# Kernel tuning notes

Measured on AMD Instinct MI355X. Metric: run time of the kernel, lower is better.

The kernel has to match this reference:

```python
import jax, jax.numpy as jnp
import numpy as np

B, NS, NC = 4096, 1024, 256
GUMBEL_HARD = True


def _linear(x, W, b):
    # torch nn.Linear: y = x @ W.T + b, W is [out, in]
    return x @ W.T + b


def _gumbel_softmax(logits, gnoise, tau, hard):
    y = jax.nn.softmax((logits + gnoise) / tau, axis=-1)
    if hard:
        y_hard = jax.nn.one_hot(jnp.argmax(y, axis=-1), y.shape[-1], dtype=y.dtype)
        y = y_hard + y - jax.lax.stop_gradient(y)  # straight-through
    return y


def setup_inputs() -> dict:
    key = jax.random.key(0)
    ks = jax.random.split(key, 32)
    inp = {
        "ct": jax.random.normal(ks[0], (B, NC), jnp.float32),
        "b1": jax.random.uniform(ks[1], (B, 2), jnp.float32),
        "b2": jax.random.uniform(ks[2], (B, 2), jnp.float32),
        "b3": jax.random.uniform(ks[3], (B, 2), jnp.float32),
        "rnn1": jax.random.normal(ks[4], (B, NS), jnp.float32),
        "rnn2": jax.random.normal(ks[5], (B, NS), jnp.float32),
        "rnn3": jax.random.normal(ks[6], (B, NS), jnp.float32),
        "rnn4": jax.random.normal(ks[7], (B, NS), jnp.float32),
        "gn1": jax.random.gumbel(ks[8], (B, 2), jnp.float32),
        "gn2": jax.random.gumbel(ks[9], (B, 2), jnp.float32),
        "gn3": jax.random.gumbel(ks[10], (B, 2), jnp.float32),
        "theta": 1,
    }
    def lin(k, out_d, in_d):
        return (0.02 * jax.random.normal(k, (out_d, in_d), jnp.float32),
                jnp.zeros((out_d,), jnp.float32))
    shapes = {
        "e_ct": (NS, NC), "rnn1_b0": (NS, 2 * NS), "rnn1_b1": (NS, 2 * NS),
        "b1_rnn1": (2, NS), "rnn2_b0": (NS, 2 * NS), "rnn2_b1": (NS, 2 * NS),
        "b2_rnn2": (2, NS), "rnn3_b0": (NS, 2 * NS), "rnn3_b1": (NS, 2 * NS),
        "b3_rnn3": (2, NS), "rnn4": (NS, 2 * NS), "hg_rnns": (NS, 4 * NS),
        "g_hg": (4, NS), "hctpi_rnns": (NS, 4 * NS), "ctpi_hctpi": (NC, NS),
    }
    for i, (name, (o, ii)) in enumerate(shapes.items()):
        W, bb = lin(ks[11 + i], o, ii)
        inp["W_" + name] = W
        inp["b_" + name] = bb
    return inp


def reference(ct, b1, b2, b3, rnn1, rnn2, rnn3, rnn4, gn1, gn2, gn3, theta,
              W_e_ct, b_e_ct, W_rnn1_b0, b_rnn1_b0, W_rnn1_b1, b_rnn1_b1,
              W_b1_rnn1, b_b1_rnn1, W_rnn2_b0, b_rnn2_b0, W_rnn2_b1, b_rnn2_b1,
              W_b2_rnn2, b_b2_rnn2, W_rnn3_b0, b_rnn3_b0, W_rnn3_b1, b_rnn3_b1,
              W_b3_rnn3, b_b3_rnn3, W_rnn4, b_rnn4, W_hg_rnns, b_hg_rnns,
              W_g_hg, b_g_hg, W_hctpi_rnns, b_hctpi_rnns, W_ctpi_hctpi, b_ctpi_hctpi):
    tau = jnp.float32(theta)
    b1tm1f = b1[:, 0:1]
    ct_e = jax.nn.relu(_linear(ct, W_e_ct, b_e_ct))

    rnn1b1 = jnp.tanh(_linear(jnp.concatenate((rnn2, ct_e), axis=1), W_rnn1_b1, b_rnn1_b1))
    rnn1b0 = jnp.tanh(_linear(jnp.concatenate((rnn1, ct_e), axis=1), W_rnn1_b0, b_rnn1_b0))
    rnn1t = b1tm1f * rnn1b1 + (1.0 - b1tm1f) * rnn1b0
    b1t = _gumbel_softmax(_linear(rnn1t, W_b1_rnn1, b_b1_rnn1), gn1, tau, GUMBEL_HARD)
    b1tf = b1t[:, 0:1]

    b2tm1f = b2[:, 0:1]
    rnn2b1 = jnp.tanh(_linear(jnp.concatenate((rnn3, rnn1t), axis=1), W_rnn2_b1, b_rnn2_b1))
    rnn2b0 = jnp.tanh(_linear(jnp.concatenate((rnn2, rnn1t), axis=1), W_rnn2_b0, b_rnn2_b0))
    rnn2_inner = (1.0 - b2tm1f) * rnn2b0 + b2tm1f * rnn2b1
    rnn2t = (1.0 - b1tf) * rnn2 + b1tf * rnn2_inner
    b2tnew = _gumbel_softmax(_linear(rnn2t, W_b2_rnn2, b_b2_rnn2), gn2, tau, GUMBEL_HARD)
    b2t = b1tf * b2tnew + (1.0 - b1tf) * b2
    b2tf = b2t[:, 0:1]

    b3tm1f = b3[:, 0:1]
    rnn3b1 = jnp.tanh(_linear(jnp.concatenate((rnn4, rnn2t), axis=1), W_rnn3_b1, b_rnn3_b1))
    rnn3b0 = jnp.tanh(_linear(jnp.concatenate((rnn3, rnn2t), axis=1), W_rnn3_b0, b_rnn3_b0))
    rnn3_inner = b3tm1f * rnn3b1 + (1.0 - b3tm1f) * rnn3b0
    rnn3t = (1.0 - b1tf) * rnn3 + b1tf * ((1.0 - b2tf) * rnn3 + b2tf * rnn3_inner)
    b3tnew = _gumbel_softmax(_linear(rnn3t, W_b3_rnn3, b_b3_rnn3), gn3, tau, GUMBEL_HARD)
    b3t = b1tf * (b2tf * b3tnew + (1.0 - b2tf) * b3) + (1.0 - b1tf) * b3
    b3tf = b3t[:, 0:1]

    rnn4_inner = jnp.tanh(_linear(jnp.concatenate((rnn4, rnn3t), axis=1), W_rnn4, b_rnn4))
    rnn4t = (1.0 - b1tf) * rnn4 + b1tf * ((1.0 - b2tf) * rnn4 + b2tf * ((1.0 - b3tf) * rnn4 + b3tf * rnn4_inner))

    hg = jax.nn.relu(_linear(jnp.concatenate((rnn1t, rnn2t, rnn3t, rnn4t), axis=1), W_hg_rnns, b_hg_rnns))
    g = jax.nn.sigmoid(_linear(hg, W_g_hg, b_g_hg))
    gated = jnp.concatenate((g[:, 0:1] * rnn1t, g[:, 1:2] * rnn2t, g[:, 2:3] * rnn3t, g[:, 3:4] * rnn4t), axis=1)
    hctpi = jax.nn.relu(_linear(gated, W_hctpi_rnns, b_hctpi_rnns))
    ctpi = jax.nn.log_softmax(_linear(hctpi, W_ctpi_hctpi, b_ctpi_hctpi), axis=1)
    return (ctpi, b1t, b2t, b3t, rnn1t, rnn2t, rnn3t, rnn4t)
```

## Files before the change

kernel.cpp:

```cpp
#include <hip/hip_runtime.h>
#include <cstdint>
#include <cstddef>

typedef unsigned short u16;
typedef __bf16 bf16x8 __attribute__((ext_vector_type(8)));
typedef float  f32x4  __attribute__((ext_vector_type(4)));

__device__ __forceinline__ void splitv(const float4 a, const float4 b, bf16x8& h, bf16x8& l) {
    float x[8] = {a.x, a.y, a.z, a.w, b.x, b.y, b.z, b.w};
#pragma unroll
    for (int i = 0; i < 8; i++) {
        __bf16 hh = (__bf16)x[i];
        h[i] = hh;
        l[i] = (__bf16)(x[i] - (float)hh);
    }
}
__device__ __forceinline__ void hiv(const float4 a, const float4 b, bf16x8& h) {
    float x[8] = {a.x, a.y, a.z, a.w, b.x, b.y, b.z, b.w};
#pragma unroll
    for (int i = 0; i < 8; i++) h[i] = (__bf16)x[i];
}

struct GemmArgs {
    const float* A0[4];
    const float* A1[4];
    const float* B0; const float* B1;
    const float* bias0; const float* bias1;
    float* Z0; float* Z1;
    int bk[4];
    int nsec, lda, ldb, N, spsl, relu, npass;
};

__global__ __launch_bounds__(256, 4) void gemm_v2(GemmArgs p) {
    __shared__ u16 Ah[128 * 32];
    __shared__ u16 Al[128 * 32];
    __shared__ u16 Bh[64 * 32];
    __shared__ u16 Bl[64 * 32];
    const int tid = threadIdx.x;
    const int lin = blockIdx.x;
    const int mt = ((lin & 7) << 2) | ((lin >> 3) & 3);
    const int nt = lin >> 5;
    const int NTh = p.N >> 6;
    const int half = (nt >= NTh) ? 1 : 0;
    const int n0 = (nt - (half ? NTh : 0)) * 64;
    const int m0 = mt * 128;
    const float* Bw  = half ? p.B1 : p.B0;
    const float* bia = half ? p.bias1 : p.bias0;
    float* Z         = half ? p.Z1 : p.Z0;
    const float* const* Asec = half ? p.A1 : p.A0;

    const int wave = tid >> 6, lane = tid & 63;
    const int quad = lane >> 4, lr = lane & 15;
    const int wm = (wave & 1) * 64, wn = (wave >> 1) * 32;
    const bool np3 = (p.npass == 3);

    f32x4 acc[4][2];
#pragma unroll
    for (int i = 0; i < 4; i++)
#pragma unroll
        for (int j = 0; j < 2; j++) acc[i][j] = (f32x4){0.f, 0.f, 0.f, 0.f};

    const int arow = tid >> 2;
    const int acol = (tid & 3) * 8;
    const size_t rA0 = (size_t)(m0 + arow) * p.lda + acol;
    const size_t rA1 = rA0 + (size_t)64 * p.lda;
    const size_t rB  = (size_t)(n0 + arow) * p.ldb + acol;
    const int sps = 1 << p.spsl;
    const int total = p.nsec << p.spsl;

    float4 v0a, v0b, v1a, v1b, vba, vbb;
    {
        const float* Ag = Asec[0];
        const float* a0 = Ag + rA0;
        const float* a1 = Ag + rA1;
        const float* b  = Bw + rB + p.bk[0];
        v0a = ((const float4*)a0)[0]; v0b = ((const float4*)a0)[1];
        v1a = ((const float4*)a1)[0]; v1b = ((const float4*)a1)[1];
        vba = ((const float4*)b)[0];  vbb = ((const float4*)b)[1];
    }

    for (int tt = 0; tt < total; ++tt) {
        __syncthreads();
        bf16x8 h, l;
        if (np3) {
            splitv(v0a, v0b, h, l);
            *(bf16x8*)&Ah[tid * 8] = h;        *(bf16x8*)&Al[tid * 8] = l;
            splitv(v1a, v1b, h, l);
            *(bf16x8*)&Ah[2048 + tid * 8] = h; *(bf16x8*)&Al[2048 + tid * 8] = l;
            splitv(vba, vbb, h, l);
            *(bf16x8*)&Bh[tid * 8] = h;        *(bf16x8*)&Bl[tid * 8] = l;
        } else {
            hiv(v0a, v0b, h); *(bf16x8*)&Ah[tid * 8] = h;
            hiv(v1a, v1b, h); *(bf16x8*)&Ah[2048 + tid * 8] = h;
            hiv(vba, vbb, h); *(bf16x8*)&Bh[tid * 8] = h;
        }
        __syncthreads();
        if (tt + 1 < total) {
            const int ts = tt + 1;
            const int s = ts >> p.spsl, t = ts & (sps - 1);
            const float* Ag = Asec[s];
            const float* a0 = Ag + rA0 + t * 32;
            const float* a1 = Ag + rA1 + t * 32;
            const float* b  = Bw + rB + p.bk[s] + t * 32;
            v0a = ((const float4*)a0)[0]; v0b = ((const float4*)a0)[1];
            v1a = ((const float4*)a1)[0]; v1b = ((const float4*)a1)[1];
            vba = ((const float4*)b)[0];  vbb = ((const float4*)b)[1];
        }
        bf16x8 ah[4], bh2[2];
#pragma unroll
        for (int i = 0; i < 4; i++)
            ah[i] = *reinterpret_cast<const bf16x8*>(&Ah[(wm + i * 16 + lr) * 32 + quad * 8]);
#pragma unroll
        for (int j = 0; j < 2; j++)
            bh2[j] = *reinterpret_cast<const bf16x8*>(&Bh[(wn + j * 16 + lr) * 32 + quad * 8]);
#pragma unroll
        for (int i = 0; i < 4; i++)
#pragma unroll
            for (int j = 0; j < 2; j++)
                acc[i][j] = __builtin_amdgcn_mfma_f32_16x16x32_bf16(ah[i], bh2[j], acc[i][j], 0, 0, 0);
        if (np3) {
            bf16x8 al[4], bl2[2];
#pragma unroll
            for (int i = 0; i < 4; i++)
                al[i] = *reinterpret_cast<const bf16x8*>(&Al[(wm + i * 16 + lr) * 32 + quad * 8]);
#pragma unroll
            for (int j = 0; j < 2; j++)
                bl2[j] = *reinterpret_cast<const bf16x8*>(&Bl[(wn + j * 16 + lr) * 32 + quad * 8]);
#pragma unroll
            for (int i = 0; i < 4; i++)
#pragma unroll
                for (int j = 0; j < 2; j++) {
                    acc[i][j] = __builtin_amdgcn_mfma_f32_16x16x32_bf16(ah[i], bl2[j], acc[i][j], 0, 0, 0);
                    acc[i][j] = __builtin_amdgcn_mfma_f32_16x16x32_bf16(al[i], bh2[j], acc[i][j], 0, 0, 0);
                }
        }
    }

#pragma unroll
    for (int j = 0; j < 2; j++) {
        const int n = n0 + wn + j * 16 + lr;
        const float bj = bia[n];
#pragma unroll
        for (int i = 0; i < 4; i++)
#pragma unroll
            for (int r = 0; r < 4; r++) {
                const int m = m0 + wm + i * 16 + quad * 4 + r;
                float v = acc[i][j][r] + bj;
                if (p.relu) v = fmaxf(v, 0.f);
                Z[(size_t)m * p.N + n] = v;
            }
    }
}

__global__ __launch_bounds__(256) void combine1(const float* Z0, const float* Z1, const float* b1in,
                                                float* outr) {
    const int base = (blockIdx.x * 256 + threadIdx.x) * 4;
    const int m = base >> 10;
    const float bf = b1in[2 * m];
    const float4 z0 = *(const float4*)(Z0 + base), z1 = *(const float4*)(Z1 + base);
    float4 o;
    o.x = bf * tanhf(z1.x) + (1.f - bf) * tanhf(z0.x);
    o.y = bf * tanhf(z1.y) + (1.f - bf) * tanhf(z0.y);
    o.z = bf * tanhf(z1.z) + (1.f - bf) * tanhf(z0.z);
    o.w = bf * tanhf(z1.w) + (1.f - bf) * tanhf(z0.w);
    *(float4*)(outr + base) = o;
}
__global__ __launch_bounds__(256) void combine2(const float* Z0, const float* Z1, const float* b2in,
                                                const float* rnn2in, const float* F1, float* outr) {
    const int base = (blockIdx.x * 256 + threadIdx.x) * 4;
    const int m = base >> 10;
    const float b2f = b2in[2 * m], f1 = F1[m];
    const float4 z0 = *(const float4*)(Z0 + base), z1 = *(const float4*)(Z1 + base);
    const float4 r2 = *(const float4*)(rnn2in + base);
    float4 o;
    o.x = (1.f - f1) * r2.x + f1 * ((1.f - b2f) * tanhf(z0.x) + b2f * tanhf(z1.x));
    o.y = (1.f - f1) * r2.y + f1 * ((1.f - b2f) * tanhf(z0.y) + b2f * tanhf(z1.y));
    o.z = (1.f - f1) * r2.z + f1 * ((1.f - b2f) * tanhf(z0.z) + b2f * tanhf(z1.z));
    o.w = (1.f - f1) * r2.w + f1 * ((1.f - b2f) * tanhf(z0.w) + b2f * tanhf(z1.w));
    *(float4*)(outr + base) = o;
}
__global__ __launch_bounds__(256) void combine3(const float* Z0, const float* Z1, const float* b3in,
                                                const float* rnn3in, const float* F1, const float* F2,
                                                float* outr) {
    const int base = (blockIdx.x * 256 + threadIdx.x) * 4;
    const int m = base >> 10;
    const float b3f = b3in[2 * m], f1 = F1[m], f2 = F2[m];
    const float4 z0 = *(const float4*)(Z0 + base), z1 = *(const float4*)(Z1 + base);
    const float4 r3 = *(const float4*)(rnn3in + base);
    float4 o;
    o.x = (1.f - f1) * r3.x + f1 * ((1.f - f2) * r3.x + f2 * (b3f * tanhf(z1.x) + (1.f - b3f) * tanhf(z0.x)));
    o.y = (1.f - f1) * r3.y + f1 * ((1.f - f2) * r3.y + f2 * (b3f * tanhf(z1.y) + (1.f - b3f) * tanhf(z0.y)));
    o.z = (1.f - f1) * r3.z + f1 * ((1.f - f2) * r3.z + f2 * (b3f * tanhf(z1.z) + (1.f - b3f) * tanhf(z0.z)));
    o.w = (1.f - f1) * r3.w + f1 * ((1.f - f2) * r3.w + f2 * (b3f * tanhf(z1.w) + (1.f - b3f) * tanhf(z0.w)));
    *(float4*)(outr + base) = o;
}
__global__ __launch_bounds__(256) void combine4(const float* Z0, const float* rnn4in, const float* F1,
                                                const float* F2, const float* F3, float* outr) {
    const int base = (blockIdx.x * 256 + threadIdx.x) * 4;
    const int m = base >> 10;
    const float f1 = F1[m], f2 = F2[m], f3 = F3[m];
    const float4 z0 = *(const float4*)(Z0 + base);
    const float4 r4 = *(const float4*)(rnn4in + base);
    float4 o;
    o.x = (1.f - f1) * r4.x + f1 * ((1.f - f2) * r4.x + f2 * ((1.f - f3) * r4.x + f3 * tanhf(z0.x)));
    o.y = (1.f - f1) * r4.y + f1 * ((1.f - f2) * r4.y + f2 * ((1.f - f3) * r4.y + f3 * tanhf(z0.y)));
    o.z = (1.f - f1) * r4.z + f1 * ((1.f - f2) * r4.z + f2 * ((1.f - f3) * r4.z + f3 * tanhf(z0.z)));
    o.w = (1.f - f1) * r4.w + f1 * ((1.f - f2) * r4.w + f2 * ((1.f - f3) * r4.w + f3 * tanhf(z0.w)));
    *(float4*)(outr + base) = o;
}

__global__ __launch_bounds__(256) void gemv_decide(const float* x, const float* W2, const float* bias2,
                                                   const float* gn, const float* bprev,
                                                   const float* Fp1, const float* Fp2,
                                                   float* bout, float* fout, int stage) {
    const int wave = threadIdx.x >> 6, lane = threadIdx.x & 63;
    const int m = blockIdx.x * 4 + wave;
    const float* row = x + (size_t)m * 1024;
    float s0 = 0.f, s1 = 0.f;
#pragma unroll 4
    for (int i = 0; i < 16; i++) {
        const int k = lane + 64 * i;
        const float v = row[k];
        s0 += v * W2[k];
        s1 += v * W2[1024 + k];
    }
    for (int off = 32; off > 0; off >>= 1) { s0 += __shfl_xor(s0, off); s1 += __shfl_xor(s1, off); }
    if (lane == 0) {
        const float l0 = s0 + bias2[0] + gn[2 * m];
        const float l1 = s1 + bias2[1] + gn[2 * m + 1];
        const float nf = (l0 >= l1) ? 1.f : 0.f;
        float v0, v1;
        if (stage == 1) {
            v0 = nf; v1 = 1.f - nf;
        } else if (stage == 2) {
            const float f1 = Fp1[m];
            const float p0 = bprev[2 * m], p1 = bprev[2 * m + 1];
            v0 = f1 * nf + (1.f - f1) * p0;
            v1 = f1 * (1.f - nf) + (1.f - f1) * p1;
        } else {
            const float f1 = Fp1[m], f2 = Fp2[m];
            const float p0 = bprev[2 * m], p1 = bprev[2 * m + 1];
            const float i0 = f2 * nf + (1.f - f2) * p0;
            const float i1 = f2 * (1.f - nf) + (1.f - f2) * p1;
            v0 = f1 * i0 + (1.f - f1) * p0;
            v1 = f1 * i1 + (1.f - f1) * p1;
        }
        fout[m] = v0;
        bout[2 * m] = v0; bout[2 * m + 1] = v1;
    }
}

__global__ __launch_bounds__(256) void gemv_g4(const float* hg, const float* Wg, const float* bg, float* G) {
    const int wave = threadIdx.x >> 6, lane = threadIdx.x & 63;
    const int m = blockIdx.x * 4 + wave;
    const float* row = hg + (size_t)m * 1024;
    float s[4] = {0.f, 0.f, 0.f, 0.f};
#pragma unroll 4
    for (int i = 0; i < 16; i++) {
        const int k = lane + 64 * i;
        const float v = row[k];
#pragma unroll
        for (int j = 0; j < 4; j++) s[j] += v * Wg[j * 1024 + k];
    }
    for (int off = 32; off > 0; off >>= 1)
#pragma unroll
        for (int j = 0; j < 4; j++) s[j] += __shfl_xor(s[j], off);
    if (lane == 0) {
#pragma unroll
        for (int j = 0; j < 4; j++) G[m * 4 + j] = 1.f / (1.f + expf(-(s[j] + bg[j])));
    }
}

__global__ __launch_bounds__(256) void gated_k(const float* rnnF, const float* G, float* gated) {
    const int base = (blockIdx.x * 256 + threadIdx.x) * 4;
    const int m = base >> 12, rem = base & 4095;
    const int j = rem >> 10, k = rem & 1023;
    const float g = G[m * 4 + j];
    const float4 r = *(const float4*)(rnnF + (size_t)j * 4194304 + (size_t)m * 1024 + k);
    float4 o; o.x = g * r.x; o.y = g * r.y; o.z = g * r.z; o.w = g * r.w;
    *(float4*)(gated + base) = o;
}

__global__ __launch_bounds__(256) void logsoftmax_k(const float* Z, float* out) {
    const int wave = threadIdx.x >> 6, lane = threadIdx.x & 63;
    const int row = blockIdx.x * 4 + wave;
    const size_t base = (size_t)row * 256;
    float x[4];
#pragma unroll
    for (int i = 0; i < 4; i++) x[i] = Z[base + lane + 64 * i];
    float mx = fmaxf(fmaxf(x[0], x[1]), fmaxf(x[2], x[3]));
    for (int off = 32; off > 0; off >>= 1) mx = fmaxf(mx, __shfl_xor(mx, off));
    float s = 0.f;
#pragma unroll
    for (int i = 0; i < 4; i++) s += expf(x[i] - mx);
    for (int off = 32; off > 0; off >>= 1) s += __shfl_xor(s, off);
    const float lse = mx + logf(s);
#pragma unroll
    for (int i = 0; i < 4; i++) out[base + lane + 64 * i] = x[i] - lse;
}

static const size_t OUT_B1 = 1048576, OUT_B2 = 1056768, OUT_B3 = 1064960;
static const size_t OUT_R1 = 1073152, OUT_R2 = 5267456, OUT_R3 = 9461760, OUT_R4 = 13656064;

extern "C" void kernel_launch(void* const* d_in, const int* in_sizes, int n_in,
                              void* d_out, int out_size, void* d_ws, size_t ws_size,
                              hipStream_t stream) {
    (void)in_sizes; (void)n_in; (void)out_size; (void)ws_size;
    const float* ct   = (const float*)d_in[0];
    const float* b1   = (const float*)d_in[1];
    const float* b2   = (const float*)d_in[2];
    const float* b3   = (const float*)d_in[3];
    const float* rnn1 = (const float*)d_in[4];
    const float* rnn2 = (const float*)d_in[5];
    const float* rnn3 = (const float*)d_in[6];
    const float* rnn4 = (const float*)d_in[7];
    const float* gn1  = (const float*)d_in[8];
    const float* gn2  = (const float*)d_in[9];
    const float* gn3  = (const float*)d_in[10];
    const float* W_e    = (const float*)d_in[12]; const float* be    = (const float*)d_in[13];
    const float* W_r1b0 = (const float*)d_in[14]; const float* br1b0 = (const float*)d_in[15];
    const float* W_r1b1 = (const float*)d_in[16]; const float* br1b1 = (const float*)d_in[17];
    const float* W_b1   = (const float*)d_in[18]; const float* bb1   = (const float*)d_in[19];
    const float* W_r2b0 = (const float*)d_in[20]; const float* br2b0 = (const float*)d_in[21];
    const float* W_r2b1 = (const float*)d_in[22]; const float* br2b1 = (const float*)d_in[23];
    const float* W_b2   = (const float*)d_in[24]; const float* bb2   = (const float*)d_in[25];
    const float* W_r3b0 = (const float*)d_in[26]; const float* br3b0 = (const float*)d_in[27];
    const float* W_r3b1 = (const float*)d_in[28]; const float* br3b1 = (const float*)d_in[29];
    const float* W_b3   = (const float*)d_in[30]; const float* bb3   = (const float*)d_in[31];
    const float* W_r4   = (const float*)d_in[32]; const float* br4   = (const float*)d_in[33];
    const float* W_hg   = (const float*)d_in[34]; const float* bhg   = (const float*)d_in[35];
    const float* W_g    = (const float*)d_in[36]; const float* bg    = (const float*)d_in[37];
    const float* W_hct  = (const float*)d_in[38]; const float* bhct  = (const float*)d_in[39];
    const float* W_ct   = (const float*)d_in[40]; const float* bct   = (const float*)d_in[41];

    float* out = (float*)d_out;
    char* w = (char*)d_ws;
    const size_t MB = 1024 * 1024;
    float* Z0    = (float*)(w + 0 * MB);
    float* Z1    = (float*)(w + 16 * MB);
    float* CTEF  = (float*)(w + 32 * MB);
    float* HGF   = (float*)(w + 48 * MB);
    float* GATED = (float*)(w + 0 * MB);
    float* HCTF  = (float*)(w + 64 * MB);
    float* ZC    = (float*)(w + 0 * MB);
    float* F1 = out; float* F2 = F1 + 4096; float* F3 = F1 + 8192; float* G4 = F1 + 12288;
    float* R1 = out + OUT_R1; float* R2 = out + OUT_R2;
    float* R3 = out + OUT_R3; float* R4 = out + OUT_R4;

    auto gemm = [&](const float* a00, const float* a01, const float* a02, const float* a03,
                    const float* a10, const float* a11,
                    const float* B0w, const float* B1w, const float* bi0, const float* bi1,
                    float* z0, float* z1, int bk1, int bk2, int bk3,
                    int nsec, int lda, int ldb, int N, int spsl, int relu, int npass, int NT) {
        GemmArgs p;
        p.A0[0] = a00; p.A0[1] = a01; p.A0[2] = a02; p.A0[3] = a03;
        p.A1[0] = a10 ? a10 : a00; p.A1[1] = a11 ? a11 : a01; p.A1[2] = a02; p.A1[3] = a03;
        p.B0 = B0w; p.B1 = B1w; p.bias0 = bi0; p.bias1 = bi1; p.Z0 = z0; p.Z1 = z1;
        p.bk[0] = 0; p.bk[1] = bk1; p.bk[2] = bk2; p.bk[3] = bk3;
        p.nsec = nsec; p.lda = lda; p.ldb = ldb; p.N = N; p.spsl = spsl;
        p.relu = relu; p.npass = npass;
        gemm_v2<<<dim3(NT * 32), 256, 0, stream>>>(p);
    };
    const dim3 EW(4096), GV(1024);

    gemm(ct, 0, 0, 0, 0, 0, W_e, W_e, be, be, CTEF, CTEF,
         0, 0, 0, 1, 256, 256, 1024, 3, 1, 3, 16);
    gemm(rnn1, CTEF, 0, 0, rnn2, CTEF, W_r1b0, W_r1b1, br1b0, br1b1, Z0, Z1,
         1024, 0, 0, 2, 1024, 2048, 1024, 5, 0, 3, 32);
    combine1<<<EW, 256, 0, stream>>>(Z0, Z1, b1, R1);
    gemv_decide<<<GV, 256, 0, stream>>>(R1, W_b1, bb1, gn1, b1, F1, F1, out + OUT_B1, F1, 1);
    gemm(rnn2, R1, 0, 0, rnn3, R1, W_r2b0, W_r2b1, br2b0, br2b1, Z0, Z1,
         1024, 0, 0, 2, 1024, 2048, 1024, 5, 0, 3, 32);
    combine2<<<EW, 256, 0, stream>>>(Z0, Z1, b2, rnn2, F1, R2);
    gemv_decide<<<GV, 256, 0, stream>>>(R2, W_b2, bb2, gn2, b2, F1, F1, out + OUT_B2, F2, 2);
    gemm(rnn3, R2, 0, 0, rnn4, R2, W_r3b0, W_r3b1, br3b0, br3b1, Z0, Z1,
         1024, 0, 0, 2, 1024, 2048, 1024, 5, 0, 3, 32);
    combine3<<<EW, 256, 0, stream>>>(Z0, Z1, b3, rnn3, F1, F2, R3);
    gemv_decide<<<GV, 256, 0, stream>>>(R3, W_b3, bb3, gn3, b3, F1, F2, out + OUT_B3, F3, 3);
    gemm(rnn4, R3, 0, 0, 0, 0, W_r4, W_r4, br4, br4, Z0, Z0,
         1024, 0, 0, 2, 1024, 2048, 1024, 5, 0, 1, 16);
    combine4<<<EW, 256, 0, stream>>>(Z0, rnn4, F1, F2, F3, R4);
    gemm(R1, R2, R3, R4, 0, 0, W_hg, W_hg, bhg, bhg, HGF, HGF,
         1024, 2048, 3072, 4, 1024, 4096, 1024, 5, 1, 1, 16);
    gemv_g4<<<GV, 256, 0, stream>>>(HGF, W_g, bg, G4);
    gated_k<<<dim3(16384), 256, 0, stream>>>(R1, G4, GATED);
    gemm(GATED, 0, 0, 0, 0, 0, W_hct, W_hct, bhct, bhct, HCTF, HCTF,
         0, 0, 0, 1, 4096, 4096, 1024, 7, 1, 1, 16);
    gemm(HCTF, 0, 0, 0, 0, 0, W_ct, W_ct, bct, bct, ZC, ZC,
         0, 0, 0, 1, 1024, 1024, 256, 5, 0, 1, 4);
    logsoftmax_k<<<GV, 256, 0, stream>>>(ZC, out);
}
```

Baseline: 1.002 ms.

## Pre-split weights and activations to bf16 hi/lo and load via global_load_lds

Adds a conversion kernel that splits fp32 weights into bf16 hi/lo arrays before each GEMM. Combine, gated and GEMM epilogues now also emit bf16 (hi/lo) copies of activations. The GEMM loads these pre-converted operands straight into swizzled LDS with global_load_lds, so it no longer converts B and most A tiles in registers every K-step and moves half the bytes. The cost is extra conversion launches and extra traffic on every call for the weights, plus a more complex mixed-mode A path.

```diff
diff --git a/kernel.cpp b/kernel.cpp
--- a/kernel.cpp
+++ b/kernel.cpp
@@ -5,6 +5,7 @@
 typedef unsigned short u16;
 typedef __bf16 bf16x8 __attribute__((ext_vector_type(8)));
 typedef float  f32x4  __attribute__((ext_vector_type(4)));
+typedef u16    u16x4  __attribute__((ext_vector_type(4)));
 
 __device__ __forceinline__ void splitv(const float4 a, const float4 b, bf16x8& h, bf16x8& l) {
     float x[8] = {a.x, a.y, a.z, a.w, b.x, b.y, b.z, b.w};
@@ -21,21 +22,32 @@
     for (int i = 0; i < 8; i++) h[i] = (__bf16)x[i];
 }
 
+__device__ __forceinline__ void gl16(const void* g, void* l) {
+    __builtin_amdgcn_global_load_lds((__attribute__((address_space(1))) void*)g,
+                                     (__attribute__((address_space(3))) void*)l, 16, 0, 0);
+}
+
+struct Sec {
+    const void* h;
+    const u16*  l;
+    int lda; int mode;
+};
 struct GemmArgs {
-    const float* A0[4];
-    const float* A1[4];
-    const float* B0; const float* B1;
+    Sec A0[4]; Sec A1[4];
+    const u16* B0h; const u16* B0l;
+    const u16* B1h; const u16* B1l;
     const float* bias0; const float* bias1;
     float* Z0; float* Z1;
+    u16* Zh0; u16* Zl0; u16* Zh1; u16* Zl1;
     int bk[4];
-    int nsec, lda, ldb, N, spsl, relu, npass;
+    int nsec, ldb, N, spsl, relu, npass, zmode;
 };
 
-__global__ __launch_bounds__(256, 4) void gemm_v2(GemmArgs p) {
-    __shared__ u16 Ah[128 * 32];
-    __shared__ u16 Al[128 * 32];
-    __shared__ u16 Bh[64 * 32];
-    __shared__ u16 Bl[64 * 32];
+__global__ __launch_bounds__(256, 4) void gemm_v3(GemmArgs p) {
+    __shared__ __align__(16) u16 Ah[128 * 32];
+    __shared__ __align__(16) u16 Al[128 * 32];
+    __shared__ __align__(16) u16 Bh[64 * 32];
+    __shared__ __align__(16) u16 Bl[64 * 32];
     const int tid = threadIdx.x;
     const int lin = blockIdx.x;
     const int mt = ((lin & 7) << 2) | ((lin >> 3) & 3);
@@ -44,10 +56,13 @@
     const int half = (nt >= NTh) ? 1 : 0;
     const int n0 = (nt - (half ? NTh : 0)) * 64;
     const int m0 = mt * 128;
-    const float* Bw  = half ? p.B1 : p.B0;
+    const u16* Bwh = half ? p.B1h : p.B0h;
+    const u16* Bwl = half ? p.B1l : p.B0l;
     const float* bia = half ? p.bias1 : p.bias0;
-    float* Z         = half ? p.Z1 : p.Z0;
-    const float* const* Asec = half ? p.A1 : p.A0;
+    float* Z = half ? p.Z1 : p.Z0;
+    u16* Zh = half ? p.Zh1 : p.Zh0;
+    u16* Zl = half ? p.Zl1 : p.Zl0;
+    const Sec* As = half ? p.A1 : p.A0;
 
     const int wave = tid >> 6, lane = tid & 63;
     const int quad = lane >> 4, lr = lane & 15;
@@ -61,58 +76,79 @@
         for (int j = 0; j < 2; j++) acc[i][j] = (f32x4){0.f, 0.f, 0.f, 0.f};
 
     const int arow = tid >> 2;
-    const int acol = (tid & 3) * 8;
-    const size_t rA0 = (size_t)(m0 + arow) * p.lda + acol;
-    const size_t rA1 = rA0 + (size_t)64 * p.lda;
-    const size_t rB  = (size_t)(n0 + arow) * p.ldb + acol;
+    const int aslot = tid & 3;
+    const int csw = aslot ^ ((arow ^ (arow >> 2)) & 3);
+    const int wr_i0 = arow * 32 + csw * 8;
+    char* AhB = (char*)Ah; char* AlB = (char*)Al;
+    char* BhB = (char*)Bh; char* BlB = (char*)Bl;
+    const int ldsw = wave * 1024;
+
+    const int qx8 = ((quad ^ ((lr ^ (lr >> 2)) & 3)) & 3) * 8;
+
     const int sps = 1 << p.spsl;
     const int total = p.nsec << p.spsl;
 
-    float4 v0a, v0b, v1a, v1b, vba, vbb;
-    {
-        const float* Ag = Asec[0];
-        const float* a0 = Ag + rA0;
-        const float* a1 = Ag + rA1;
-        const float* b  = Bw + rB + p.bk[0];
-        v0a = ((const float4*)a0)[0]; v0b = ((const float4*)a0)[1];
-        v1a = ((const float4*)a1)[0]; v1b = ((const float4*)a1)[1];
-        vba = ((const float4*)b)[0];  vbb = ((const float4*)b)[1];
+    float4 v0a{}, v0b{}, v1a{}, v1b{};
+    {
+        const Sec s0 = As[0];
+        if (s0.mode == 0) {
+            const float* a0 = (const float*)s0.h + (size_t)(m0 + arow) * s0.lda + aslot * 8;
+            v0a = ((const float4*)a0)[0]; v0b = ((const float4*)a0)[1];
+            const float* a1 = a0 + (size_t)64 * s0.lda;
+            v1a = ((const float4*)a1)[0]; v1b = ((const float4*)a1)[1];
+        }
     }
 
     for (int tt = 0; tt < total; ++tt) {
+        const int s = tt >> p.spsl, t = tt & (sps - 1);
         __syncthreads();
-        bf16x8 h, l;
-        if (np3) {
-            splitv(v0a, v0b, h, l);
-            *(bf16x8*)&Ah[tid * 8] = h;        *(bf16x8*)&Al[tid * 8] = l;
-            splitv(v1a, v1b, h, l);
-            *(bf16x8*)&Ah[2048 + tid * 8] = h; *(bf16x8*)&Al[2048 + tid * 8] = l;
-            splitv(vba, vbb, h, l);
-            *(bf16x8*)&Bh[tid * 8] = h;        *(bf16x8*)&Bl[tid * 8] = l;
+        {
+            const size_t off = (size_t)(n0 + arow) * p.ldb + p.bk[s] + t * 32 + csw * 8;
+            gl16(Bwh + off, BhB + ldsw);
+            if (np3) gl16(Bwl + off, BlB + ldsw);
+        }
+        const Sec sec = As[s];
+        if (sec.mode == 0) {
+            if (np3) {
+                bf16x8 h, l;
+                splitv(v0a, v0b, h, l);
+                *(bf16x8*)&Ah[wr_i0] = h;        *(bf16x8*)&Al[wr_i0] = l;
+                splitv(v1a, v1b, h, l);
+                *(bf16x8*)&Ah[2048 + wr_i0] = h; *(bf16x8*)&Al[2048 + wr_i0] = l;
+            } else {
+                bf16x8 h;
+                hiv(v0a, v0b, h); *(bf16x8*)&Ah[wr_i0] = h;
+                hiv(v1a, v1b, h); *(bf16x8*)&Ah[2048 + wr_i0] = h;
+            }
         } else {
-            hiv(v0a, v0b, h); *(bf16x8*)&Ah[tid * 8] = h;
-            hiv(v1a, v1b, h); *(bf16x8*)&Ah[2048 + tid * 8] = h;
-            hiv(vba, vbb, h); *(bf16x8*)&Bh[tid * 8] = h;
+            const u16* gh = (const u16*)sec.h;
+            const size_t o0 = (size_t)(m0 + arow) * sec.lda + t * 32 + csw * 8;
+            const size_t o1 = o0 + (size_t)64 * sec.lda;
+            gl16(gh + o0, AhB + ldsw);
+            gl16(gh + o1, AhB + 4096 + ldsw);
+            if (np3) {
+                gl16(sec.l + o0, AlB + ldsw);
+                gl16(sec.l + o1, AlB + 4096 + ldsw);
+            }
         }
         __syncthreads();
         if (tt + 1 < total) {
-            const int ts = tt + 1;
-            const int s = ts >> p.spsl, t = ts & (sps - 1);
-            const float* Ag = Asec[s];
-            const float* a0 = Ag + rA0 + t * 32;
-            const float* a1 = Ag + rA1 + t * 32;
-            const float* b  = Bw + rB + p.bk[s] + t * 32;
-            v0a = ((const float4*)a0)[0]; v0b = ((const float4*)a0)[1];
-            v1a = ((const float4*)a1)[0]; v1b = ((const float4*)a1)[1];
-            vba = ((const float4*)b)[0];  vbb = ((const float4*)b)[1];
+            const int s2 = (tt + 1) >> p.spsl, t2 = (tt + 1) & (sps - 1);
+            const Sec sn = As[s2];
+            if (sn.mode == 0) {
+                const float* a0 = (const float*)sn.h + (size_t)(m0 + arow) * sn.lda + t2 * 32 + aslot * 8;
+                v0a = ((const float4*)a0)[0]; v0b = ((const float4*)a0)[1];
+                const float* a1 = a0 + (size_t)64 * sn.lda;
+                v1a = ((const float4*)a1)[0]; v1b = ((const float4*)a1)[1];
+            }
         }
         bf16x8 ah[4], bh2[2];
 #pragma unroll
         for (int i = 0; i < 4; i++)
-            ah[i] = *reinterpret_cast<const bf16x8*>(&Ah[(wm + i * 16 + lr) * 32 + quad * 8]);
+            ah[i] = *reinterpret_cast<const bf16x8*>(&Ah[(wm + i * 16 + lr) * 32 + qx8]);
 #pragma unroll
         for (int j = 0; j < 2; j++)
-            bh2[j] = *reinterpret_cast<const bf16x8*>(&Bh[(wn + j * 16 + lr) * 32 + quad * 8]);
+            bh2[j] = *reinterpret_cast<const bf16x8*>(&Bh[(wn + j * 16 + lr) * 32 + qx8]);
 #pragma unroll
         for (int i = 0; i < 4; i++)
 #pragma unroll
@@ -122,10 +158,10 @@
             bf16x8 al[4], bl2[2];
 #pragma unroll
             for (int i = 0; i < 4; i++)
-                al[i] = *reinterpret_cast<const bf16x8*>(&Al[(wm + i * 16 + lr) * 32 + quad * 8]);
+                al[i] = *reinterpret_cast<const bf16x8*>(&Al[(wm + i * 16 + lr) * 32 + qx8]);
 #pragma unroll
             for (int j = 0; j < 2; j++)
-                bl2[j] = *reinterpret_cast<const bf16x8*>(&Bl[(wn + j * 16 + lr) * 32 + quad * 8]);
+                bl2[j] = *reinterpret_cast<const bf16x8*>(&Bl[(wn + j * 16 + lr) * 32 + qx8]);
 #pragma unroll
             for (int i = 0; i < 4; i++)
 #pragma unroll
@@ -147,13 +183,46 @@
                 const int m = m0 + wm + i * 16 + quad * 4 + r;
                 float v = acc[i][j][r] + bj;
                 if (p.relu) v = fmaxf(v, 0.f);
-                Z[(size_t)m * p.N + n] = v;
+                const size_t zi = (size_t)m * p.N + n;
+                if (p.zmode == 0) {
+                    Z[zi] = v;
+                } else {
+                    __bf16 hb = (__bf16)v;
+                    Zh[zi] = __builtin_bit_cast(u16, hb);
+                    if (p.zmode == 2)
+                        Zl[zi] = __builtin_bit_cast(u16, (__bf16)(v - (float)hb));
+                }
             }
     }
 }
 
+__global__ __launch_bounds__(256) void conv_split(const float* x0, u16* h0, u16* l0, int n0v,
+                                                  const float* x1, u16* h1, u16* l1, int n1v) {
+    int i = blockIdx.x * 256 + threadIdx.x;
+    const float* x; u16* h; u16* l;
+    if (i < n0v) { x = x0; h = h0; l = l0; }
+    else { i -= n0v; if (i >= n1v) return; x = x1; h = h1; l = l1; }
+    const float4 a = ((const float4*)x)[2 * i], b = ((const float4*)x)[2 * i + 1];
+    bf16x8 hh, ll;
+    if (l) { splitv(a, b, hh, ll); ((bf16x8*)h)[i] = hh; ((bf16x8*)l)[i] = ll; }
+    else   { hiv(a, b, hh);        ((bf16x8*)h)[i] = hh; }
+}
+
+__device__ __forceinline__ void store_hl4(const float4 o, u16* hp, u16* lp, int base) {
+    float xs[4] = {o.x, o.y, o.z, o.w};
+    u16x4 hv, lv;
+#pragma unroll
+    for (int k = 0; k < 4; k++) {
+        __bf16 hb = (__bf16)xs[k];
+        hv[k] = __builtin_bit_cast(u16, hb);
+        if (lp) lv[k] = __builtin_bit_cast(u16, (__bf16)(xs[k] - (float)hb));
+    }
+    *(u16x4*)(hp + base) = hv;
+    if (lp) *(u16x4*)(lp + base) = lv;
+}
+
 __global__ __launch_bounds__(256) void combine1(const float* Z0, const float* Z1, const float* b1in,
-                                                float* outr) {
+                                                float* outr, u16* hO, u16* lO) {
     const int base = (blockIdx.x * 256 + threadIdx.x) * 4;
     const int m = base >> 10;
     const float bf = b1in[2 * m];
@@ -164,9 +233,11 @@
     o.z = bf * tanhf(z1.z) + (1.f - bf) * tanhf(z0.z);
     o.w = bf * tanhf(z1.w) + (1.f - bf) * tanhf(z0.w);
     *(float4*)(outr + base) = o;
+    store_hl4(o, hO, lO, base);
 }
 __global__ __launch_bounds__(256) void combine2(const float* Z0, const float* Z1, const float* b2in,
-                                                const float* rnn2in, const float* F1, float* outr) {
+                                                const float* rnn2in, const float* F1, float* outr,
+                                                u16* hO, u16* lO) {
     const int base = (blockIdx.x * 256 + threadIdx.x) * 4;
     const int m = base >> 10;
     const float b2f = b2in[2 * m], f1 = F1[m];
@@ -178,10 +249,11 @@
     o.z = (1.f - f1) * r2.z + f1 * ((1.f - b2f) * tanhf(z0.z) + b2f * tanhf(z1.z));
     o.w = (1.f - f1) * r2.w + f1 * ((1.f - b2f) * tanhf(z0.w) + b2f * tanhf(z1.w));
     *(float4*)(outr + base) = o;
+    store_hl4(o, hO, lO, base);
 }
 __global__ __launch_bounds__(256) void combine3(const float* Z0, const float* Z1, const float* b3in,
                                                 const float* rnn3in, const float* F1, const float* F2,
-                                                float* outr) {
+                                                float* outr, u16* hO) {
     const int base = (blockIdx.x * 256 + threadIdx.x) * 4;
     const int m = base >> 10;
     const float b3f = b3in[2 * m], f1 = F1[m], f2 = F2[m];
@@ -193,9 +265,10 @@
     o.z = (1.f - f1) * r3.z + f1 * ((1.f - f2) * r3.z + f2 * (b3f * tanhf(z1.z) + (1.f - b3f) * tanhf(z0.z)));
     o.w = (1.f - f1) * r3.w + f1 * ((1.f - f2) * r3.w + f2 * (b3f * tanhf(z1.w) + (1.f - b3f) * tanhf(z0.w)));
     *(float4*)(outr + base) = o;
+    store_hl4(o, hO, nullptr, base);
 }
 __global__ __launch_bounds__(256) void combine4(const float* Z0, const float* rnn4in, const float* F1,
-                                                const float* F2, const float* F3, float* outr) {
+                                                const float* F2, const float* F3, float* outr, u16* hO) {
     const int base = (blockIdx.x * 256 + threadIdx.x) * 4;
     const int m = base >> 10;
     const float f1 = F1[m], f2 = F2[m], f3 = F3[m];
@@ -207,6 +280,7 @@
     o.z = (1.f - f1) * r4.z + f1 * ((1.f - f2) * r4.z + f2 * ((1.f - f3) * r4.z + f3 * tanhf(z0.z)));
     o.w = (1.f - f1) * r4.w + f1 * ((1.f - f2) * r4.w + f2 * ((1.f - f3) * r4.w + f3 * tanhf(z0.w)));
     *(float4*)(outr + base) = o;
+    store_hl4(o, hO, nullptr, base);
 }
 
 __global__ __launch_bounds__(256) void gemv_decide(const float* x, const float* W2, const float* bias2,
@@ -271,14 +345,18 @@
     }
 }
 
-__global__ __launch_bounds__(256) void gated_k(const float* rnnF, const float* G, float* gated) {
+__global__ __launch_bounds__(256) void gated_k(const float* rnnF, const float* G, u16* gatedh) {
     const int base = (blockIdx.x * 256 + threadIdx.x) * 4;
     const int m = base >> 12, rem = base & 4095;
     const int j = rem >> 10, k = rem & 1023;
     const float g = G[m * 4 + j];
     const float4 r = *(const float4*)(rnnF + (size_t)j * 4194304 + (size_t)m * 1024 + k);
-    float4 o; o.x = g * r.x; o.y = g * r.y; o.z = g * r.z; o.w = g * r.w;
-    *(float4*)(gated + base) = o;
+    u16x4 hv;
+    hv[0] = __builtin_bit_cast(u16, (__bf16)(g * r.x));
+    hv[1] = __builtin_bit_cast(u16, (__bf16)(g * r.y));
+    hv[2] = __builtin_bit_cast(u16, (__bf16)(g * r.z));
+    hv[3] = __builtin_bit_cast(u16, (__bf16)(g * r.w));
+    *(u16x4*)(gatedh + base) = hv;
 }
 
 __global__ __launch_bounds__(256) void logsoftmax_k(const float* Z, float* out) {
@@ -301,6 +379,9 @@
 
 static const size_t OUT_B1 = 1048576, OUT_B2 = 1056768, OUT_B3 = 1064960;
 static const size_t OUT_R1 = 1073152, OUT_R2 = 5267456, OUT_R3 = 9461760, OUT_R4 = 13656064;
+
+static inline Sec S0(const float* f, int lda) { Sec s; s.h = f; s.l = nullptr; s.lda = lda; s.mode = 0; return s; }
+static inline Sec S1(const u16* h, const u16* l, int lda) { Sec s; s.h = h; s.l = l; s.lda = lda; s.mode = 1; return s; }
 
 extern "C" void kernel_launch(void* const* d_in, const int* in_sizes, int n_in,
                               void* d_out, int out_size, void* d_ws, size_t ws_size,
@@ -336,57 +417,136 @@
     float* out = (float*)d_out;
     char* w = (char*)d_ws;
     const size_t MB = 1024 * 1024;
-    float* Z0    = (float*)(w + 0 * MB);
+    float* Z0    = (float*)(w);
     float* Z1    = (float*)(w + 16 * MB);
-    float* CTEF  = (float*)(w + 32 * MB);
-    float* HGF   = (float*)(w + 48 * MB);
-    float* GATED = (float*)(w + 0 * MB);
-    float* HCTF  = (float*)(w + 64 * MB);
-    float* ZC    = (float*)(w + 0 * MB);
+    u16* WS      = (u16*)(w + 32 * MB);
+    u16* CTEFh   = (u16*)(w + 48 * MB);
+    u16* CTEFl   = (u16*)(w + 56 * MB);
+    u16* R1h     = (u16*)(w + 64 * MB);
+    u16* R1l     = (u16*)(w + 72 * MB);
+    u16* R2h     = (u16*)(w + 48 * MB);
+    u16* R2l     = (u16*)(w + 56 * MB);
+    u16* R3h     = (u16*)(w + 72 * MB);
+    u16* R4h     = (u16*)(w + 56 * MB);
+    float* HGF   = (float*)(w);
+    u16* GATEDh  = (u16*)(w);
+    u16* HCTFh   = (u16*)(w + 48 * MB);
+    float* ZC    = (float*)(w);
     float* F1 = out; float* F2 = F1 + 4096; float* F3 = F1 + 8192; float* G4 = F1 + 12288;
     float* R1 = out + OUT_R1; float* R2 = out + OUT_R2;
     float* R3 = out + OUT_R3; float* R4 = out + OUT_R4;
 
-    auto gemm = [&](const float* a00, const float* a01, const float* a02, const float* a03,
-                    const float* a10, const float* a11,
-                    const float* B0w, const float* B1w, const float* bi0, const float* bi1,
-                    float* z0, float* z1, int bk1, int bk2, int bk3,
-                    int nsec, int lda, int ldb, int N, int spsl, int relu, int npass, int NT) {
-        GemmArgs p;
-        p.A0[0] = a00; p.A0[1] = a01; p.A0[2] = a02; p.A0[3] = a03;
-        p.A1[0] = a10 ? a10 : a00; p.A1[1] = a11 ? a11 : a01; p.A1[2] = a02; p.A1[3] = a03;
-        p.B0 = B0w; p.B1 = B1w; p.bias0 = bi0; p.bias1 = bi1; p.Z0 = z0; p.Z1 = z1;
-        p.bk[0] = 0; p.bk[1] = bk1; p.bk[2] = bk2; p.bk[3] = bk3;
-        p.nsec = nsec; p.lda = lda; p.ldb = ldb; p.N = N; p.spsl = spsl;
-        p.relu = relu; p.npass = npass;
-        gemm_v2<<<dim3(NT * 32), 256, 0, stream>>>(p);
+    const int NWe = 32768, NWr = 262144, NWg = 524288, NWct = 32768;
+    auto conv = [&](const float* x0, u16* h0, u16* l0, int n0v,
+                    const float* x1, u16* h1, u16* l1, int n1v) {
+        const int tot = n0v + n1v;
+        conv_split<<<dim3((tot + 255) / 256), 256, 0, stream>>>(x0, h0, l0, n0v, x1, h1, l1, n1v);
     };
     const dim3 EW(4096), GV(1024);
 
-    gemm(ct, 0, 0, 0, 0, 0, W_e, W_e, be, be, CTEF, CTEF,
-         0, 0, 0, 1, 256, 256, 1024, 3, 1, 3, 16);
-    gemm(rnn1, CTEF, 0, 0, rnn2, CTEF, W_r1b0, W_r1b1, br1b0, br1b1, Z0, Z1,
-         1024, 0, 0, 2, 1024, 2048, 1024, 5, 0, 3, 32);
-    combine1<<<EW, 256, 0, stream>>>(Z0, Z1, b1, R1);
+    conv(W_e, WS, WS + 262144, NWe, nullptr, nullptr, nullptr, 0);
+    {
+        GemmArgs p{};
+        p.A0[0] = S0(ct, 256); p.A1[0] = p.A0[0];
+        p.B0h = WS; p.B0l = WS + 262144; p.B1h = p.B0h; p.B1l = p.B0l;
+        p.bias0 = be; p.bias1 = be;
+        p.Zh0 = CTEFh; p.Zl0 = CTEFl; p.Zh1 = CTEFh; p.Zl1 = CTEFl;
+        p.bk[0] = 0; p.nsec = 1; p.ldb = 256; p.N = 1024; p.spsl = 3;
+        p.relu = 1; p.npass = 3; p.zmode = 2;
+        gemm_v3<<<dim3(16 * 32), 256, 0, stream>>>(p);
+    }
+    conv(W_r1b0, WS, WS + 2097152, NWr, W_r1b1, WS + 4194304, WS + 6291456, NWr);
+    {
+        GemmArgs p{};
+        p.A0[0] = S0(rnn1, 1024); p.A0[1] = S1(CTEFh, CTEFl, 1024);
+        p.A1[0] = S0(rnn2, 1024); p.A1[1] = p.A0[1];
+        p.B0h = WS; p.B0l = WS + 2097152; p.B1h = WS + 4194304; p.B1l = WS + 6291456;
+        p.bias0 = br1b0; p.bias1 = br1b1;
+        p.Z0 = Z0; p.Z1 = Z1;
+        p.bk[0] = 0; p.bk[1] = 1024; p.nsec = 2; p.ldb = 2048; p.N = 1024; p.spsl = 5;
+        p.relu = 0; p.npass = 3; p.zmode = 0;
+        gemm_v3<<<dim3(32 * 32), 256, 0, stream>>>(p);
+    }
+    combine1<<<EW, 256, 0, stream>>>(Z0, Z1, b1, R1, R1h, R1l);
     gemv_decide<<<GV, 256, 0, stream>>>(R1, W_b1, bb1, gn1, b1, F1, F1, out + OUT_B1, F1, 1);
-    gemm(rnn2, R1, 0, 0, rnn3, R1, W_r2b0, W_r2b1, br2b0, br2b1, Z0, Z1,
-         1024, 0, 0, 2, 1024, 2048, 1024, 5, 0, 3, 32);
-    combine2<<<EW, 256, 0, stream>>>(Z0, Z1, b2, rnn2, F1, R2);
+    conv(W_r2b0, WS, WS + 2097152, NWr, W_r2b1, WS + 4194304, WS + 6291456, NWr);
+    {
+        GemmArgs p{};
+        p.A0[0] = S0(rnn2, 1024); p.A0[1] = S1(R1h, R1l, 1024);
+        p.A1[0] = S0(rnn3, 1024); p.A1[1] = p.A0[1];
+        p.B0h = WS; p.B0l = WS + 2097152; p.B1h = WS + 4194304; p.B1l = WS + 6291456;
+        p.bias0 = br2b0; p.bias1 = br2b1;
+        p.Z0 = Z0; p.Z1 = Z1;
+        p.bk[0] = 0; p.bk[1] = 1024; p.nsec = 2; p.ldb = 2048; p.N = 1024; p.spsl = 5;
+        p.relu = 0; p.npass = 3; p.zmode = 0;
+        gemm_v3<<<dim3(32 * 32), 256, 0, stream>>>(p);
+    }
+    combine2<<<EW, 256, 0, stream>>>(Z0, Z1, b2, rnn2, F1, R2, R2h, R2l);
     gemv_decide<<<GV, 256, 0, stream>>>(R2, W_b2, bb2, gn2, b2, F1, F1, out + OUT_B2, F2, 2);
-    gemm(rnn3, R2, 0, 0, rnn4, R2, W_r3b0, W_r3b1, br3b0, br3b1, Z0, Z1,
-         1024, 0, 0, 2, 1024, 2048, 1024, 5, 0, 3, 32);
-    combine3<<<EW, 256, 0, stream>>>(Z0, Z1, b3, rnn3, F1, F2, R3);
+    conv(W_r3b0, WS, WS + 2097152, NWr, W_r3b1, WS + 4194304, WS + 6291456, NWr);
+    {
+        GemmArgs p{};
+        p.A0[0] = S0(rnn3, 1024); p.A0[1] = S1(R2h, R2l, 1024);
+        p.A1[0] = S0(rnn4, 1024); p.A1[1] = p.A0[1];
+        p.B0h = WS; p.B0l = WS + 2097152; p.B1h = WS + 4194304; p.B1l = WS + 6291456;
+        p.bias0 = br3b0; p.bias1 = br3b1;
+        p.Z0 = Z0; p.Z1 = Z1;
+        p.bk[0] = 0; p.bk[1] = 1024; p.nsec = 2; p.ldb = 2048; p.N = 1024; p.spsl = 5;
+        p.relu = 0; p.npass = 3; p.zmode = 0;
+        gemm_v3<<<dim3(32 * 32), 256, 0, stream>>>(p);
+    }
+    combine3<<<EW, 256, 0, stream>>>(Z0, Z1, b3, rnn3, F1, F2, R3, R3h);
     gemv_decide<<<GV, 256, 0, stream>>>(R3, W_b3, bb3, gn3, b3, F1, F2, out + OUT_B3, F3, 3);
-    gemm(rnn4, R3, 0, 0, 0, 0, W_r4, W_r4, br4, br4, Z0, Z0,
-         1024, 0, 0, 2, 1024, 2048, 1024, 5, 0, 1, 16);
-    combine4<<<EW, 256, 0, stream>>>(Z0, rnn4, F1, F2, F3, R4);
-    gemm(R1, R2, R3, R4, 0, 0, W_hg, W_hg, bhg, bhg, HGF, HGF,
-         1024, 2048, 3072, 4, 1024, 4096, 1024, 5, 1, 1, 16);
+    conv(W_r4, WS, nullptr, NWr, nullptr, nullptr, nullptr, 0);
+    {
+        GemmArgs p{};
+        p.A0[0] = S0(rnn4, 1024); p.A0[1] = S1(R3h, nullptr, 1024);
+        p.A1[0] = p.A0[0]; p.A1[1] = p.A0[1];
+        p.B0h = WS; p.B0l = nullptr; p.B1h = WS; p.B1l = nullptr;
+        p.bias0 = br4; p.bias1 = br4;
+        p.Z0 = Z0; p.Z1 = Z0;
+        p.bk[0] = 0; p.bk[1] = 1024; p.nsec = 2; p.ldb = 2048; p.N = 1024; p.spsl = 5;
+        p.relu = 0; p.npass = 1; p.zmode = 0;
+        gemm_v3<<<dim3(16 * 32), 256, 0, stream>>>(p);
+    }
+    combine4<<<EW, 256, 0, stream>>>(Z0, rnn4, F1, F2, F3, R4, R4h);
+    conv(W_hg, WS, nullptr, NWg, nullptr, nullptr, nullptr, 0);
+    {
+        GemmArgs p{};
+        p.A0[0] = S1(R1h, nullptr, 1024); p.A0[1] = S1(R2h, nullptr, 1024);
+        p.A0[2] = S1(R3h, nullptr, 1024); p.A0[3] = S1(R4h, nullptr, 1024);
+        p.A1[0] = p.A0[0]; p.A1[1] = p.A0[1]; p.A1[2] = p.A0[2]; p.A1[3] = p.A0[3];
+        p.B0h = WS; p.B1h = WS;
+        p.bias0 = bhg; p.bias1 = bhg;
+        p.Z0 = HGF; p.Z1 = HGF;
+        p.bk[0] = 0; p.bk[1] = 1024; p.bk[2] = 2048; p.bk[3] = 3072;
+        p.nsec = 4; p.ldb = 4096; p.N = 1024; p.spsl = 5;
+        p.relu = 1; p.npass = 1; p.zmode = 0;
+        gemm_v3<<<dim3(16 * 32), 256, 0, stream>>>(p);
+    }
     gemv_g4<<<GV, 256, 0, stream>>>(HGF, W_g, bg, G4);
-    gated_k<<<dim3(16384), 256, 0, stream>>>(R1, G4, GATED);
-    gemm(GATED, 0, 0, 0, 0, 0, W_hct, W_hct, bhct, bhct, HCTF, HCTF,
-         0, 0, 0, 1, 4096, 4096, 1024, 7, 1, 1, 16);
-    gemm(HCTF, 0, 0, 0, 0, 0, W_ct, W_ct, bct, bct, ZC, ZC,
-         0, 0, 0, 1, 1024, 1024, 256, 5, 0, 1, 4);
+    gated_k<<<dim3(16384), 256, 0, stream>>>(R1, G4, GATEDh);
+    conv(W_hct, WS, nullptr, NWg, nullptr, nullptr, nullptr, 0);
+    {
+        GemmArgs p{};
+        p.A0[0] = S1(GATEDh, nullptr, 4096); p.A1[0] = p.A0[0];
+        p.B0h = WS; p.B1h = WS;
+        p.bias0 = bhct; p.bias1 = bhct;
+        p.Zh0 = HCTFh; p.Zh1 = HCTFh;
+        p.bk[0] = 0; p.nsec = 1; p.ldb = 4096; p.N = 1024; p.spsl = 7;
+        p.relu = 1; p.npass = 1; p.zmode = 1;
+        gemm_v3<<<dim3(16 * 32), 256, 0, stream>>>(p);
+    }
+    conv(W_ct, WS, nullptr, NWct, nullptr, nullptr, nullptr, 0);
+    {
+        GemmArgs p{};
+        p.A0[0] = S1(HCTFh, nullptr, 1024); p.A1[0] = p.A0[0];
+        p.B0h = WS; p.B1h = WS;
+        p.bias0 = bct; p.bias1 = bct;
+        p.Z0 = ZC; p.Z1 = ZC;
+        p.bk[0] = 0; p.nsec = 1; p.ldb = 1024; p.N = 256; p.spsl = 5;
+        p.relu = 0; p.npass = 1; p.zmode = 0;
+        gemm_v3<<<dim3(4 * 32), 256, 0, stream>>>(p);
+    }
     logsoftmax_k<<<GV, 256, 0, stream>>>(ZC, out);
 }
```

After: 946.7 us. 1.06x faster.
